# Kernel optimization log

Measured on AMD Instinct MI355X. Metric: run time of the kernel, lower is better.

Reference implementation:

```python
import jax, jax.numpy as jnp
import numpy as np

B, S, DIN, DQ, DK = 8, 2048, 1024, 64, 64

def setup_inputs() -> dict:
    key = jax.random.key(0)
    ks = jax.random.split(key, 8)
    sc = 0.02
    return {
        "input_tensor": jax.random.normal(ks[0], (B, S, DIN), jnp.float32),
        "attention_mask": jax.random.randint(ks[1], (B, 1, S), 0, 2) == 1,
        "Wq": jax.random.normal(ks[2], (DIN, DQ), jnp.float32) * sc,
        "bq": jnp.zeros((DQ,), jnp.float32),
        "Wk": jax.random.normal(ks[3], (DIN, DK), jnp.float32) * sc,
        "bk": jnp.zeros((DK,), jnp.float32),
        "Wv": jax.random.normal(ks[4], (DIN, DK), jnp.float32) * sc,
        "bv": jnp.zeros((DK,), jnp.float32),
    }

def reference(input_tensor, attention_mask, Wq, bq, Wk, bk, Wv, bv):
    q = input_tensor @ Wq + bq          # [B,S,DQ]
    k = input_tensor @ Wk + bk          # [B,S,DK]
    v = input_tensor @ Wv + bv          # [B,S,DK]
    # NOTE: original scales by sqrt(query.size(1)) == sqrt(seq_len), faithfully kept
    scale = q.shape[1] ** 0.5
    scores = jnp.einsum('bqd,bkd->bqk', q, k) / scale
    scores = jnp.where(attention_mask, jnp.float32(-1e9), scores)
    attn = jax.nn.softmax(scores, axis=-1)
    context = jnp.einsum('bqk,bkd->bqd', attn, v)
    return context
```

## Files before the change

### kernel.cpp

```cpp
#include <hip/hip_runtime.h>
#include <hip/hip_bf16.h>

#define NB 8
#define SEQ 2048
#define DIN 1024
#define DH 64

typedef __attribute__((ext_vector_type(8))) short bf16x8;
typedef __attribute__((ext_vector_type(4))) float f32x4;

static __device__ __forceinline__ unsigned short f2bf(float f) {
    unsigned int u = __builtin_bit_cast(unsigned int, f);
    unsigned int r = (u + 0x7FFFu + ((u >> 16) & 1u)) >> 16;
    return (unsigned short)r;
}

__global__ __launch_bounds__(256) void prep_kernel(
    const float* __restrict__ Wq, const float* __restrict__ Wk, const float* __restrict__ Wv,
    const int* __restrict__ mask, unsigned short* __restrict__ Wfrag, float* __restrict__ bias)
{
    int i = blockIdx.x * 256 + threadIdx.x;
    if (i < 3 * DH * DIN) {
        int cg = i >> 14;
        int kk = (i >> 9) & 31;
        int e  = i & 511;
        int cl = e >> 5;
        int kq = (e >> 3) & 3;
        int ke = e & 7;
        int col = cg * 16 + cl;
        int mat = col >> 6, c = col & 63;
        int k = kk * 32 + kq * 8 + ke;
        const float* W = (mat == 0) ? Wq : ((mat == 1) ? Wk : Wv);
        Wfrag[i] = f2bf(W[k * DH + c]);
    } else {
        int j = i - 3 * DH * DIN;
        if (j < NB * SEQ) bias[j] = mask[j] ? -1e30f : 0.0f;
    }
}

#define QBK 128

__global__ __launch_bounds__(256, 4) void qkv_kernel(
    const float* __restrict__ X, const unsigned short* __restrict__ Wfrag,
    const float* __restrict__ bq, const float* __restrict__ bk, const float* __restrict__ bv,
    unsigned short* __restrict__ Qb, unsigned short* __restrict__ Kb, unsigned short* __restrict__ Vt)
{
    __shared__ __align__(16) short As[32][QBK];

    const int tid = threadIdx.x;
    const int w   = tid >> 6;
    const int l   = tid & 63;
    const int l15 = l & 15;
    const int lq  = l >> 4;
    const int row0 = blockIdx.x * 32;

    f32x4 acc[2][3] = {};

    const int srow = tid >> 3;
    const int scg  = (tid & 7) * 16;
    const float* xb = X + (size_t)(row0 + srow) * DIN + scg;
    const int swcol0 = (scg)     ^ ((srow & 7) << 3);
    const int swcol1 = (scg + 8) ^ ((srow & 7) << 3);

    const unsigned short* wfb[3];
    #pragma unroll
    for (int n = 0; n < 3; ++n)
        wfb[n] = Wfrag + (size_t)((w * 3 + n) * 32) * 512 + (l15 * 4 + lq) * 8;

    float4 pf0 = *(const float4*)(xb + 0);
    float4 pf1 = *(const float4*)(xb + 4);
    float4 pf2 = *(const float4*)(xb + 8);
    float4 pf3 = *(const float4*)(xb + 12);

    for (int step = 0; step < DIN / QBK; ++step) {
        bf16x8 sv0, sv1;
        sv0[0] = (short)f2bf(pf0.x); sv0[1] = (short)f2bf(pf0.y);
        sv0[2] = (short)f2bf(pf0.z); sv0[3] = (short)f2bf(pf0.w);
        sv0[4] = (short)f2bf(pf1.x); sv0[5] = (short)f2bf(pf1.y);
        sv0[6] = (short)f2bf(pf1.z); sv0[7] = (short)f2bf(pf1.w);
        sv1[0] = (short)f2bf(pf2.x); sv1[1] = (short)f2bf(pf2.y);
        sv1[2] = (short)f2bf(pf2.z); sv1[3] = (short)f2bf(pf2.w);
        sv1[4] = (short)f2bf(pf3.x); sv1[5] = (short)f2bf(pf3.y);
        sv1[6] = (short)f2bf(pf3.z); sv1[7] = (short)f2bf(pf3.w);

        if (step < DIN / QBK - 1) {
            const float* xn = xb + (step + 1) * QBK;
            pf0 = *(const float4*)(xn + 0);
            pf1 = *(const float4*)(xn + 4);
            pf2 = *(const float4*)(xn + 8);
            pf3 = *(const float4*)(xn + 12);
        }

        __syncthreads();
        *(bf16x8*)&As[srow][swcol0] = sv0;
        *(bf16x8*)&As[srow][swcol1] = sv1;
        __syncthreads();

        #pragma unroll
        for (int kkl = 0; kkl < 4; ++kkl) {
            int kk = step * 4 + kkl;
            bf16x8 bfr[3];
            #pragma unroll
            for (int n = 0; n < 3; ++n)
                bfr[n] = *(const bf16x8*)(wfb[n] + kk * 512);
            bf16x8 a[2];
            #pragma unroll
            for (int m = 0; m < 2; ++m) {
                int row = m * 16 + l15;
                int col = (kkl * 32 + lq * 8) ^ ((row & 7) << 3);
                a[m] = *(const bf16x8*)&As[row][col];
            }
            #pragma unroll
            for (int m = 0; m < 2; ++m)
                #pragma unroll
                for (int n = 0; n < 3; ++n)
                    acc[m][n] = __builtin_amdgcn_mfma_f32_16x16x32_bf16(a[m], bfr[n], acc[m][n], 0, 0, 0);
        }
    }

    #pragma unroll
    for (int n = 0; n < 3; ++n) {
        int col = w * 48 + n * 16 + l15;
        int mat = col >> 6, c = col & 63;
        float badd = ((mat == 0) ? bq : ((mat == 1) ? bk : bv))[c];
        #pragma unroll
        for (int m = 0; m < 2; ++m) {
            #pragma unroll
            for (int reg = 0; reg < 4; ++reg) {
                int row = row0 + m * 16 + lq * 4 + reg;
                unsigned short v16 = f2bf(acc[m][n][reg] + badd);
                if (mat == 0)      Qb[(size_t)row * DH + c] = v16;
                else if (mat == 1) Kb[(size_t)row * DH + c] = v16;
                else {
                    int bb = row >> 11, ss = row & 2047;
                    Vt[((size_t)(bb * DH + c)) * SEQ + ss] = v16;
                }
            }
        }
    }
}

#define KT 128
#define NT (SEQ / KT)

__global__ __launch_bounds__(256, 2) void attn_kernel(
    const unsigned short* __restrict__ Qb, const unsigned short* __restrict__ Kb,
    const unsigned short* __restrict__ Vt, const float* __restrict__ bias,
    float* __restrict__ out)
{
    __shared__ __align__(16) short Ks[2][KT][DH];
    __shared__ __align__(16) short Vs[2][DH][KT];
    __shared__ __align__(16) short ps[128][40];
    __shared__ float sml[4][32];

    const int tid = threadIdx.x;
    const int w   = tid >> 6;
    const int l   = tid & 63;
    const int l15 = l & 15;
    const int lq  = l >> 4;

    int bid = blockIdx.x;
    bid = (bid & 7) * 64 + (bid >> 3);
    const int b  = bid >> 6;
    const int q0 = (bid & 63) * 32;

    bf16x8 aq[2][2];
    #pragma unroll
    for (int m = 0; m < 2; ++m)
        #pragma unroll
        for (int kk = 0; kk < 2; ++kk)
            aq[m][kk] = *(const bf16x8*)(Qb + ((size_t)(b * SEQ + q0 + m * 16 + l15)) * DH + kk * 32 + lq * 8);

    const int krow = tid >> 3;
    const int kcolb = (tid & 7) * 16;
    const int kdst = (kcolb ^ ((krow & 7) << 4)) >> 1;
    const int vrow = tid >> 4;
    const int vcolb = (tid & 15) * 16;
    const int vdst = (vcolb ^ ((vrow & 7) << 4)) >> 1;

    const unsigned short* Kbase = Kb + (size_t)(b * SEQ) * DH + (kcolb >> 1);
    const unsigned short* Vbase = Vt + (size_t)(b * DH) * SEQ + (vcolb >> 1) - 0;

    bf16x8 kr[4], vr[4];
    #pragma unroll
    for (int i = 0; i < 4; ++i) {
        kr[i] = *(const bf16x8*)(Kbase + (size_t)(i * 32 + krow) * DH);
        vr[i] = *(const bf16x8*)(Vt + ((size_t)(b * DH + i * 16 + vrow)) * SEQ + (vcolb >> 1));
    }

    f32x4 o[2][4];
    #pragma unroll
    for (int m = 0; m < 2; ++m)
        #pragma unroll
        for (int n = 0; n < 4; ++n) o[m][n] = f32x4{0, 0, 0, 0};
    float lr[2][4] = {};

    const float rscale = 0.022097086912079612f;
    const int kw = w * 32;

    for (int t = 0; t < NT; ++t) {
        const int cur = t & 1;

        #pragma unroll
        for (int i = 0; i < 4; ++i) *(bf16x8*)&Ks[cur][i * 32 + krow][kdst] = kr[i];
        #pragma unroll
        for (int i = 0; i < 4; ++i) *(bf16x8*)&Vs[cur][i * 16 + vrow][vdst] = vr[i];

        if (t + 1 < NT) {
            const int key0n = (t + 1) * KT;
            #pragma unroll
            for (int i = 0; i < 4; ++i) {
                kr[i] = *(const bf16x8*)(Kbase + (size_t)(key0n + i * 32 + krow) * DH);
                vr[i] = *(const bf16x8*)(Vt + ((size_t)(b * DH + i * 16 + vrow)) * SEQ + key0n + (vcolb >> 1));
            }
        }

        __syncthreads();

        bf16x8 bkf[2][2];
        #pragma unroll
        for (int n = 0; n < 2; ++n)
            #pragma unroll
            for (int kk = 0; kk < 2; ++kk) {
                int col = (kk * 32 + lq * 8) ^ ((l15 & 7) << 3);
                bkf[n][kk] = *(const bf16x8*)&Ks[cur][kw + n * 16 + l15][col];
            }
        f32x4 s[2][2];
        #pragma unroll
        for (int m = 0; m < 2; ++m)
            #pragma unroll
            for (int n = 0; n < 2; ++n) s[m][n] = f32x4{0, 0, 0, 0};
        #pragma unroll
        for (int kk = 0; kk < 2; ++kk)
            #pragma unroll
            for (int m = 0; m < 2; ++m)
                #pragma unroll
                for (int n = 0; n < 2; ++n)
                    s[m][n] = __builtin_amdgcn_mfma_f32_16x16x32_bf16(aq[m][kk], bkf[n][kk], s[m][n], 0, 0, 0);

        float bb0 = bias[b * SEQ + t * KT + kw + l15];
        float bb1 = bias[b * SEQ + t * KT + kw + 16 + l15];
        #pragma unroll
        for (int m = 0; m < 2; ++m)
            #pragma unroll
            for (int n = 0; n < 2; ++n) {
                float bvv = n ? bb1 : bb0;
                #pragma unroll
                for (int r = 0; r < 4; ++r) {
                    float p = __expf(fmaf(s[m][n][r], rscale, bvv));
                    lr[m][r] += p;
                    ps[w * 32 + m * 16 + lq * 4 + r][n * 16 + l15] = (short)f2bf(p);
                }
            }

        bf16x8 pa[2];
        #pragma unroll
        for (int m = 0; m < 2; ++m)
            pa[m] = *(const bf16x8*)&ps[w * 32 + m * 16 + l15][lq * 8];
        bf16x8 bvf[4];
        #pragma unroll
        for (int n = 0; n < 4; ++n) {
            int col = (kw + lq * 8) ^ ((l15 & 7) << 3);
            bvf[n] = *(const bf16x8*)&Vs[cur][n * 16 + l15][col];
        }
        #pragma unroll
        for (int m = 0; m < 2; ++m)
            #pragma unroll
            for (int n = 0; n < 4; ++n)
                o[m][n] = __builtin_amdgcn_mfma_f32_16x16x32_bf16(pa[m], bvf[n], o[m][n], 0, 0, 0);
    }

    #pragma unroll
    for (int off = 1; off < 16; off <<= 1)
        #pragma unroll
        for (int m = 0; m < 2; ++m)
            #pragma unroll
            for (int r = 0; r < 4; ++r) lr[m][r] += __shfl_xor(lr[m][r], off);
    if (l15 == 0) {
        #pragma unroll
        for (int m = 0; m < 2; ++m)
            #pragma unroll
            for (int r = 0; r < 4; ++r) sml[w][m * 16 + lq * 4 + r] = lr[m][r];
    }
    __syncthreads();

    float (*so)[32][64] = reinterpret_cast<float (*)[32][64]>(&Ks[0][0][0]);
    #pragma unroll
    for (int m = 0; m < 2; ++m)
        #pragma unroll
        for (int n = 0; n < 4; ++n)
            #pragma unroll
            for (int r = 0; r < 4; ++r)
                so[w][m * 16 + lq * 4 + r][n * 16 + l15] = o[m][n][r];
    __syncthreads();

    {
        int q  = tid >> 3;
        int d0 = (tid & 7) * 8;
        float lt = sml[0][q] + sml[1][q] + sml[2][q] + sml[3][q];
        float inv = 1.0f / lt;
        float vx[8];
        #pragma unroll
        for (int j = 0; j < 8; ++j)
            vx[j] = (so[0][q][d0 + j] + so[1][q][d0 + j] + so[2][q][d0 + j] + so[3][q][d0 + j]) * inv;
        float* op = out + ((size_t)(b * SEQ + q0 + q)) * DH + d0;
        float4 r0; r0.x = vx[0]; r0.y = vx[1]; r0.z = vx[2]; r0.w = vx[3];
        float4 r1; r1.x = vx[4]; r1.y = vx[5]; r1.z = vx[6]; r1.w = vx[7];
        *(float4*)op = r0;
        *(float4*)(op + 4) = r1;
    }
}

extern "C" void kernel_launch(void* const* d_in, const int* in_sizes, int n_in,
                              void* d_out, int out_size, void* d_ws, size_t ws_size,
                              hipStream_t stream) {
    const float* X    = (const float*)d_in[0];
    const int*   mask = (const int*)d_in[1];
    const float* Wq   = (const float*)d_in[2];
    const float* bq   = (const float*)d_in[3];
    const float* Wk   = (const float*)d_in[4];
    const float* bk   = (const float*)d_in[5];
    const float* Wv   = (const float*)d_in[6];
    const float* bv   = (const float*)d_in[7];
    float* out = (float*)d_out;

    char* ws = (char*)d_ws;
    unsigned short* Qb = (unsigned short*)(ws);
    unsigned short* Kb = (unsigned short*)(ws + (2u << 20));
    unsigned short* Vt = (unsigned short*)(ws + (4u << 20));
    unsigned short* Wfrag = (unsigned short*)(ws + (6u << 20));
    float* bias        = (float*)(ws + (6u << 20) + 3 * DH * DIN * 2);

    prep_kernel<<<832, 256, 0, stream>>>(Wq, Wk, Wv, mask, Wfrag, bias);
    qkv_kernel<<<512, 256, 0, stream>>>(X, Wfrag, bq, bk, bv, Qb, Kb, Vt);
    attn_kernel<<<512, 256, 0, stream>>>(Qb, Kb, Vt, bias, out);
}
```

Measured before the change: 55.74 us.

## Retile QKV and attention kernels, read mask directly, use packed bf16 convert

```diff
diff --git a/kernel.cpp b/kernel.cpp
--- a/kernel.cpp
+++ b/kernel.cpp
@@ -15,205 +15,194 @@
     return (unsigned short)r;
 }
 
+static __device__ __forceinline__ unsigned int cvt_pk_bf16(float lo, float hi) {
+    unsigned int d;
+    asm volatile("v_cvt_pk_bf16_f32 %0, %1, %2" : "=v"(d) : "v"(lo), "v"(hi));
+    return d;
+}
+
 __global__ __launch_bounds__(256) void prep_kernel(
     const float* __restrict__ Wq, const float* __restrict__ Wk, const float* __restrict__ Wv,
-    const int* __restrict__ mask, unsigned short* __restrict__ Wfrag, float* __restrict__ bias)
+    unsigned short* __restrict__ Wfrag)
 {
-    int i = blockIdx.x * 256 + threadIdx.x;
-    if (i < 3 * DH * DIN) {
-        int cg = i >> 14;
-        int kk = (i >> 9) & 31;
-        int e  = i & 511;
-        int cl = e >> 5;
-        int kq = (e >> 3) & 3;
-        int ke = e & 7;
-        int col = cg * 16 + cl;
-        int mat = col >> 6, c = col & 63;
-        int k = kk * 32 + kq * 8 + ke;
-        const float* W = (mat == 0) ? Wq : ((mat == 1) ? Wk : Wv);
-        Wfrag[i] = f2bf(W[k * DH + c]);
-    } else {
-        int j = i - 3 * DH * DIN;
-        if (j < NB * SEQ) bias[j] = mask[j] ? -1e30f : 0.0f;
-    }
-}
-
-#define QBK 128
+    int j = blockIdx.x * 256 + threadIdx.x;
+    int mat = j >> 16;
+    int rem = j & 65535;
+    int k = rem >> 6;
+    int c = rem & 63;
+    const float* W = (mat == 0) ? Wq : ((mat == 1) ? Wk : Wv);
+    float v = W[rem];
+    int col = mat * 64 + c;
+    int cg = col >> 4, cl = col & 15;
+    int kk = k >> 5, kq = (k >> 3) & 3, ke = k & 7;
+    Wfrag[(size_t)(cg * 32 + kk) * 512 + cl * 32 + kq * 8 + ke] = f2bf(v);
+}
 
 __global__ __launch_bounds__(256, 4) void qkv_kernel(
     const float* __restrict__ X, const unsigned short* __restrict__ Wfrag,
     const float* __restrict__ bq, const float* __restrict__ bk, const float* __restrict__ bv,
     unsigned short* __restrict__ Qb, unsigned short* __restrict__ Kb, unsigned short* __restrict__ Vt)
 {
-    __shared__ __align__(16) short As[32][QBK];
+    __shared__ __align__(16) short As[16][128];
+
+    const int tid = threadIdx.x;
+    const int w   = tid >> 6;
+    const int l15 = tid & 15;
+    const int lq  = (tid & 63) >> 4;
+    const int row0 = blockIdx.x * 16;
+
+    f32x4 acc[3] = {};
+
+    const int srow = tid >> 4;
+    const int scol = (tid & 15) * 8;
+    const float* xb = X + (size_t)(row0 + srow) * DIN + scol;
+    const int swc = scol ^ ((srow & 7) << 3);
+
+    const unsigned short* wfb[3];
+    #pragma unroll
+    for (int n = 0; n < 3; ++n)
+        wfb[n] = Wfrag + (size_t)((w * 3 + n) * 32) * 512 + (l15 * 4 + lq) * 8;
+
+    float4 pa0 = *(const float4*)(xb);
+    float4 pa1 = *(const float4*)(xb + 4);
+    float4 pb0 = *(const float4*)(xb + 128);
+    float4 pb1 = *(const float4*)(xb + 132);
+
+    #pragma unroll
+    for (int step = 0; step < 8; ++step) {
+        float4 c0 = (step & 1) ? pb0 : pa0;
+        float4 c1 = (step & 1) ? pb1 : pa1;
+        unsigned int u0 = cvt_pk_bf16(c0.x, c0.y);
+        unsigned int u1 = cvt_pk_bf16(c0.z, c0.w);
+        unsigned int u2 = cvt_pk_bf16(c1.x, c1.y);
+        unsigned int u3 = cvt_pk_bf16(c1.z, c1.w);
+
+        if (step + 2 < 8) {
+            const float* xn = xb + (step + 2) * 128;
+            if (step & 1) { pb0 = *(const float4*)(xn); pb1 = *(const float4*)(xn + 4); }
+            else          { pa0 = *(const float4*)(xn); pa1 = *(const float4*)(xn + 4); }
+        }
+
+        __syncthreads();
+        uint4 pk; pk.x = u0; pk.y = u1; pk.z = u2; pk.w = u3;
+        *(uint4*)&As[srow][swc] = pk;
+        __syncthreads();
+
+        #pragma unroll
+        for (int kkl = 0; kkl < 4; ++kkl) {
+            bf16x8 bfr[3];
+            #pragma unroll
+            for (int n = 0; n < 3; ++n)
+                bfr[n] = *(const bf16x8*)(wfb[n] + (size_t)(step * 4 + kkl) * 512);
+            bf16x8 a = *(const bf16x8*)&As[l15][(kkl * 32 + lq * 8) ^ ((l15 & 7) << 3)];
+            #pragma unroll
+            for (int n = 0; n < 3; ++n)
+                acc[n] = __builtin_amdgcn_mfma_f32_16x16x32_bf16(a, bfr[n], acc[n], 0, 0, 0);
+        }
+    }
+
+    #pragma unroll
+    for (int n = 0; n < 3; ++n) {
+        int col = w * 48 + n * 16 + l15;
+        int mat = col >> 6, c = col & 63;
+        float badd = ((mat == 0) ? bq : ((mat == 1) ? bk : bv))[c];
+        #pragma unroll
+        for (int reg = 0; reg < 4; ++reg) {
+            int row = row0 + lq * 4 + reg;
+            unsigned short v16 = f2bf(acc[n][reg] + badd);
+            if (mat == 0)      Qb[(size_t)row * DH + c] = v16;
+            else if (mat == 1) Kb[(size_t)row * DH + c] = v16;
+            else {
+                int bb = row >> 11, ss = row & 2047;
+                Vt[((size_t)(bb * DH + c)) * SEQ + ss] = v16;
+            }
+        }
+    }
+}
+
+#define KT 128
+#define NT (SEQ / KT)
+#define PPITCH 36
+
+__global__ __launch_bounds__(512, 2) void attn_kernel(
+    const unsigned short* __restrict__ Qb, const unsigned short* __restrict__ Kb,
+    const unsigned short* __restrict__ Vt, const int* __restrict__ mask,
+    float* __restrict__ out)
+{
+    __shared__ __align__(16) unsigned char smem[65536 + 8 * 32 * PPITCH * 2 + 8 * 32 * 4];
+    short (*Ks)[KT][DH]     = reinterpret_cast<short (*)[KT][DH]>(smem);
+    short (*Vs)[DH][KT]     = reinterpret_cast<short (*)[DH][KT]>(smem + 32768);
+    short (*ps)[32][PPITCH] = reinterpret_cast<short (*)[32][PPITCH]>(smem + 65536);
+    float (*sml)[32]        = reinterpret_cast<float (*)[32]>(smem + 65536 + 8 * 32 * PPITCH * 2);
+    float (*so)[64][64]     = reinterpret_cast<float (*)[64][64]>(smem);
 
     const int tid = threadIdx.x;
     const int w   = tid >> 6;
     const int l   = tid & 63;
     const int l15 = l & 15;
     const int lq  = l >> 4;
-    const int row0 = blockIdx.x * 32;
-
-    f32x4 acc[2][3] = {};
-
-    const int srow = tid >> 3;
-    const int scg  = (tid & 7) * 16;
-    const float* xb = X + (size_t)(row0 + srow) * DIN + scg;
-    const int swcol0 = (scg)     ^ ((srow & 7) << 3);
-    const int swcol1 = (scg + 8) ^ ((srow & 7) << 3);
-
-    const unsigned short* wfb[3];
-    #pragma unroll
-    for (int n = 0; n < 3; ++n)
-        wfb[n] = Wfrag + (size_t)((w * 3 + n) * 32) * 512 + (l15 * 4 + lq) * 8;
-
-    float4 pf0 = *(const float4*)(xb + 0);
-    float4 pf1 = *(const float4*)(xb + 4);
-    float4 pf2 = *(const float4*)(xb + 8);
-    float4 pf3 = *(const float4*)(xb + 12);
-
-    for (int step = 0; step < DIN / QBK; ++step) {
-        bf16x8 sv0, sv1;
-        sv0[0] = (short)f2bf(pf0.x); sv0[1] = (short)f2bf(pf0.y);
-        sv0[2] = (short)f2bf(pf0.z); sv0[3] = (short)f2bf(pf0.w);
-        sv0[4] = (short)f2bf(pf1.x); sv0[5] = (short)f2bf(pf1.y);
-        sv0[6] = (short)f2bf(pf1.z); sv0[7] = (short)f2bf(pf1.w);
-        sv1[0] = (short)f2bf(pf2.x); sv1[1] = (short)f2bf(pf2.y);
-        sv1[2] = (short)f2bf(pf2.z); sv1[3] = (short)f2bf(pf2.w);
-        sv1[4] = (short)f2bf(pf3.x); sv1[5] = (short)f2bf(pf3.y);
-        sv1[6] = (short)f2bf(pf3.z); sv1[7] = (short)f2bf(pf3.w);
-
-        if (step < DIN / QBK - 1) {
-            const float* xn = xb + (step + 1) * QBK;
-            pf0 = *(const float4*)(xn + 0);
-            pf1 = *(const float4*)(xn + 4);
-            pf2 = *(const float4*)(xn + 8);
-            pf3 = *(const float4*)(xn + 12);
-        }
-
-        __syncthreads();
-        *(bf16x8*)&As[srow][swcol0] = sv0;
-        *(bf16x8*)&As[srow][swcol1] = sv1;
-        __syncthreads();
-
-        #pragma unroll
-        for (int kkl = 0; kkl < 4; ++kkl) {
-            int kk = step * 4 + kkl;
-            bf16x8 bfr[3];
-            #pragma unroll
-            for (int n = 0; n < 3; ++n)
-                bfr[n] = *(const bf16x8*)(wfb[n] + kk * 512);
-            bf16x8 a[2];
-            #pragma unroll
-            for (int m = 0; m < 2; ++m) {
-                int row = m * 16 + l15;
-                int col = (kkl * 32 + lq * 8) ^ ((row & 7) << 3);
-                a[m] = *(const bf16x8*)&As[row][col];
-            }
-            #pragma unroll
-            for (int m = 0; m < 2; ++m)
-                #pragma unroll
-                for (int n = 0; n < 3; ++n)
-                    acc[m][n] = __builtin_amdgcn_mfma_f32_16x16x32_bf16(a[m], bfr[n], acc[m][n], 0, 0, 0);
-        }
-    }
-
-    #pragma unroll
-    for (int n = 0; n < 3; ++n) {
-        int col = w * 48 + n * 16 + l15;
-        int mat = col >> 6, c = col & 63;
-        float badd = ((mat == 0) ? bq : ((mat == 1) ? bk : bv))[c];
-        #pragma unroll
-        for (int m = 0; m < 2; ++m) {
-            #pragma unroll
-            for (int reg = 0; reg < 4; ++reg) {
-                int row = row0 + m * 16 + lq * 4 + reg;
-                unsigned short v16 = f2bf(acc[m][n][reg] + badd);
-                if (mat == 0)      Qb[(size_t)row * DH + c] = v16;
-                else if (mat == 1) Kb[(size_t)row * DH + c] = v16;
-                else {
-                    int bb = row >> 11, ss = row & 2047;
-                    Vt[((size_t)(bb * DH + c)) * SEQ + ss] = v16;
-                }
+    const int wqh = w >> 2;
+    const int wkq = w & 3;
+
+    int bid = blockIdx.x;
+    bid = (bid & 7) * 32 + (bid >> 3);
+    const int b  = bid >> 5;
+    const int q0 = (bid & 31) * 64;
+
+    bf16x8 aq[2][2];
+    #pragma unroll
+    for (int m = 0; m < 2; ++m)
+        #pragma unroll
+        for (int kk = 0; kk < 2; ++kk)
+            aq[m][kk] = *(const bf16x8*)(Qb + ((size_t)(b * SEQ + q0 + wqh * 32 + m * 16 + l15)) * DH + kk * 32 + lq * 8);
+
+    const int krow = tid >> 3;
+    const int kcol = (tid & 7) * 8;
+    const int kdst = kcol ^ ((krow & 7) << 3);
+    const int vrow = tid >> 4;
+    const int vcol = (tid & 15) * 8;
+    const int vdst = vcol ^ ((vrow & 7) << 3);
+
+    const unsigned short* Kbase = Kb + (size_t)(b * SEQ) * DH + kcol;
+    const unsigned short* Vbase = Vt + (size_t)(b * DH) * SEQ + vcol;
+
+    bf16x8 kr[2], vr[2];
+    #pragma unroll
+    for (int i = 0; i < 2; ++i) {
+        kr[i] = *(const bf16x8*)(Kbase + (size_t)(i * 64 + krow) * DH);
+        vr[i] = *(const bf16x8*)(Vbase + (size_t)(i * 32 + vrow) * SEQ);
+    }
+
+    f32x4 o[2][4];
+    #pragma unroll
+    for (int m = 0; m < 2; ++m)
+        #pragma unroll
+        for (int n = 0; n < 4; ++n) o[m][n] = f32x4{0, 0, 0, 0};
+    float lr[2][4] = {};
+
+    const float rscale = 0.022097086912079612f;
+    const int kw = wkq * 32;
+    const int* mbase = mask + b * SEQ + kw + l15;
+
+    for (int t = 0; t < NT; ++t) {
+        const int cur = t & 1;
+
+        #pragma unroll
+        for (int i = 0; i < 2; ++i) *(bf16x8*)&Ks[cur][i * 64 + krow][kdst] = kr[i];
+        #pragma unroll
+        for (int i = 0; i < 2; ++i) *(bf16x8*)&Vs[cur][i * 32 + vrow][vdst] = vr[i];
+
+        int mk0 = mbase[t * KT];
+        int mk1 = mbase[t * KT + 16];
+
+        if (t + 1 < NT) {
+            const int key0n = (t + 1) * KT;
+            #pragma unroll
+            for (int i = 0; i < 2; ++i) {
+                kr[i] = *(const bf16x8*)(Kbase + (size_t)(key0n + i * 64 + krow) * DH);
+                vr[i] = *(const bf16x8*)(Vbase + (size_t)(i * 32 + vrow) * SEQ + key0n);
             }
         }
-    }
-}
-
-#define KT 128
-#define NT (SEQ / KT)
-
-__global__ __launch_bounds__(256, 2) void attn_kernel(
-    const unsigned short* __restrict__ Qb, const unsigned short* __restrict__ Kb,
-    const unsigned short* __restrict__ Vt, const float* __restrict__ bias,
-    float* __restrict__ out)
-{
-    __shared__ __align__(16) short Ks[2][KT][DH];
-    __shared__ __align__(16) short Vs[2][DH][KT];
-    __shared__ __align__(16) short ps[128][40];
-    __shared__ float sml[4][32];
-
-    const int tid = threadIdx.x;
-    const int w   = tid >> 6;
-    const int l   = tid & 63;
-    const int l15 = l & 15;
-    const int lq  = l >> 4;
-
-    int bid = blockIdx.x;
-    bid = (bid & 7) * 64 + (bid >> 3);
-    const int b  = bid >> 6;
-    const int q0 = (bid & 63) * 32;
-
-    bf16x8 aq[2][2];
-    #pragma unroll
-    for (int m = 0; m < 2; ++m)
-        #pragma unroll
-        for (int kk = 0; kk < 2; ++kk)
-            aq[m][kk] = *(const bf16x8*)(Qb + ((size_t)(b * SEQ + q0 + m * 16 + l15)) * DH + kk * 32 + lq * 8);
-
-    const int krow = tid >> 3;
-    const int kcolb = (tid & 7) * 16;
-    const int kdst = (kcolb ^ ((krow & 7) << 4)) >> 1;
-    const int vrow = tid >> 4;
-    const int vcolb = (tid & 15) * 16;
-    const int vdst = (vcolb ^ ((vrow & 7) << 4)) >> 1;
-
-    const unsigned short* Kbase = Kb + (size_t)(b * SEQ) * DH + (kcolb >> 1);
-    const unsigned short* Vbase = Vt + (size_t)(b * DH) * SEQ + (vcolb >> 1) - 0;
-
-    bf16x8 kr[4], vr[4];
-    #pragma unroll
-    for (int i = 0; i < 4; ++i) {
-        kr[i] = *(const bf16x8*)(Kbase + (size_t)(i * 32 + krow) * DH);
-        vr[i] = *(const bf16x8*)(Vt + ((size_t)(b * DH + i * 16 + vrow)) * SEQ + (vcolb >> 1));
-    }
-
-    f32x4 o[2][4];
-    #pragma unroll
-    for (int m = 0; m < 2; ++m)
-        #pragma unroll
-        for (int n = 0; n < 4; ++n) o[m][n] = f32x4{0, 0, 0, 0};
-    float lr[2][4] = {};
-
-    const float rscale = 0.022097086912079612f;
-    const int kw = w * 32;
-
-    for (int t = 0; t < NT; ++t) {
-        const int cur = t & 1;
-
-        #pragma unroll
-        for (int i = 0; i < 4; ++i) *(bf16x8*)&Ks[cur][i * 32 + krow][kdst] = kr[i];
-        #pragma unroll
-        for (int i = 0; i < 4; ++i) *(bf16x8*)&Vs[cur][i * 16 + vrow][vdst] = vr[i];
-
-        if (t + 1 < NT) {
-            const int key0n = (t + 1) * KT;
-            #pragma unroll
-            for (int i = 0; i < 4; ++i) {
-                kr[i] = *(const bf16x8*)(Kbase + (size_t)(key0n + i * 32 + krow) * DH);
-                vr[i] = *(const bf16x8*)(Vt + ((size_t)(b * DH + i * 16 + vrow)) * SEQ + key0n + (vcolb >> 1));
-            }
-        }
 
         __syncthreads();
 
@@ -221,10 +210,8 @@
         #pragma unroll
         for (int n = 0; n < 2; ++n)
             #pragma unroll
-            for (int kk = 0; kk < 2; ++kk) {
-                int col = (kk * 32 + lq * 8) ^ ((l15 & 7) << 3);
-                bkf[n][kk] = *(const bf16x8*)&Ks[cur][kw + n * 16 + l15][col];
-            }
+            for (int kk = 0; kk < 2; ++kk)
+                bkf[n][kk] = *(const bf16x8*)&Ks[cur][kw + n * 16 + l15][(kk * 32 + lq * 8) ^ ((l15 & 7) << 3)];
         f32x4 s[2][2];
         #pragma unroll
         for (int m = 0; m < 2; ++m)
@@ -238,8 +225,8 @@
                 for (int n = 0; n < 2; ++n)
                     s[m][n] = __builtin_amdgcn_mfma_f32_16x16x32_bf16(aq[m][kk], bkf[n][kk], s[m][n], 0, 0, 0);
 
-        float bb0 = bias[b * SEQ + t * KT + kw + l15];
-        float bb1 = bias[b * SEQ + t * KT + kw + 16 + l15];
+        float bb0 = mk0 ? -1e30f : 0.0f;
+        float bb1 = mk1 ? -1e30f : 0.0f;
         #pragma unroll
         for (int m = 0; m < 2; ++m)
             #pragma unroll
@@ -249,20 +236,18 @@
                 for (int r = 0; r < 4; ++r) {
                     float p = __expf(fmaf(s[m][n][r], rscale, bvv));
                     lr[m][r] += p;
-                    ps[w * 32 + m * 16 + lq * 4 + r][n * 16 + l15] = (short)f2bf(p);
+                    ps[w][m * 16 + lq * 4 + r][n * 16 + l15] = (short)f2bf(p);
                 }
             }
 
         bf16x8 pa[2];
         #pragma unroll
         for (int m = 0; m < 2; ++m)
-            pa[m] = *(const bf16x8*)&ps[w * 32 + m * 16 + l15][lq * 8];
+            pa[m] = *(const bf16x8*)&ps[w][m * 16 + l15][lq * 8];
         bf16x8 bvf[4];
         #pragma unroll
-        for (int n = 0; n < 4; ++n) {
-            int col = (kw + lq * 8) ^ ((l15 & 7) << 3);
-            bvf[n] = *(const bf16x8*)&Vs[cur][n * 16 + l15][col];
-        }
+        for (int n = 0; n < 4; ++n)
+            bvf[n] = *(const bf16x8*)&Vs[cur][n * 16 + l15][(kw + lq * 8) ^ ((l15 & 7) << 3)];
         #pragma unroll
         for (int m = 0; m < 2; ++m)
             #pragma unroll
@@ -284,20 +269,20 @@
     }
     __syncthreads();
 
-    float (*so)[32][64] = reinterpret_cast<float (*)[32][64]>(&Ks[0][0][0]);
     #pragma unroll
     for (int m = 0; m < 2; ++m)
         #pragma unroll
         for (int n = 0; n < 4; ++n)
             #pragma unroll
             for (int r = 0; r < 4; ++r)
-                so[w][m * 16 + lq * 4 + r][n * 16 + l15] = o[m][n][r];
+                so[wkq][wqh * 32 + m * 16 + lq * 4 + r][n * 16 + l15] = o[m][n][r];
     __syncthreads();
 
     {
         int q  = tid >> 3;
         int d0 = (tid & 7) * 8;
-        float lt = sml[0][q] + sml[1][q] + sml[2][q] + sml[3][q];
+        int wb = (q >> 5) * 4;
+        float lt = sml[wb][q & 31] + sml[wb + 1][q & 31] + sml[wb + 2][q & 31] + sml[wb + 3][q & 31];
         float inv = 1.0f / lt;
         float vx[8];
         #pragma unroll
@@ -329,9 +314,8 @@
     unsigned short* Kb = (unsigned short*)(ws + (2u << 20));
     unsigned short* Vt = (unsigned short*)(ws + (4u << 20));
     unsigned short* Wfrag = (unsigned short*)(ws + (6u << 20));
-    float* bias        = (float*)(ws + (6u << 20) + 3 * DH * DIN * 2);
-
-    prep_kernel<<<832, 256, 0, stream>>>(Wq, Wk, Wv, mask, Wfrag, bias);
-    qkv_kernel<<<512, 256, 0, stream>>>(X, Wfrag, bq, bk, bv, Qb, Kb, Vt);
-    attn_kernel<<<512, 256, 0, stream>>>(Qb, Kb, Vt, bias, out);
-}
+
+    prep_kernel<<<768, 256, 0, stream>>>(Wq, Wk, Wv, Wfrag);
+    qkv_kernel<<<1024, 256, 0, stream>>>(X, Wfrag, bq, bk, bv, Qb, Kb, Vt);
+    attn_kernel<<<256, 512, 0, stream>>>(Qb, Kb, Vt, mask, out);
+}
```

Measured after the change: 66.98 us. 20.2% more time.
